# Optimization experiments

Measured on AMD Instinct MI355X. Metric: run time of the kernel, lower is better.

Reference implementation:

```python
import jax, jax.numpy as jnp
import numpy as np

NQ = 4          # QUANTUM_QUBITS
DIM = 2 ** NQ   # 16-dim statevector
N_LAYERS = 2
BATCH = 1 << 20


def _bit(idx, w):
    # PennyLane convention: wire 0 is the most-significant bit
    return (idx >> (NQ - 1 - w)) & 1

# Precompute CNOT permutations for the ring (w, (w+1)%NQ): flip target bit when control bit is 1.
_CNOT_PERMS = []
for w in range(NQ):
    c, t = w, (w + 1) % NQ
    perm = np.arange(DIM)
    for idx in range(DIM):
        if _bit(idx, c):
            perm[idx] = idx ^ (1 << (NQ - 1 - t))
    _CNOT_PERMS.append(jnp.asarray(perm))

# Z expectation sign vectors: sign = +1 if bit==0 else -1, per wire -> (NQ, DIM)
_Z_SIGNS = jnp.asarray(
    np.stack([[1.0 - 2.0 * _bit(idx, w) for idx in range(DIM)] for w in range(NQ)]),
    dtype=jnp.float32,
)


def _ry(t):
    c, s = jnp.cos(t / 2), jnp.sin(t / 2)
    return jnp.stack([jnp.stack([c, -s], -1), jnp.stack([s, c], -1)], -2).astype(jnp.complex64)


def _rx(t):
    c = jnp.cos(t / 2).astype(jnp.complex64)
    s = (-1j * jnp.sin(t / 2)).astype(jnp.complex64)
    return jnp.stack([jnp.stack([c, s], -1), jnp.stack([s, c], -1)], -2)


def _rz(t):
    em = jnp.exp(-0.5j * t.astype(jnp.complex64))
    ep = jnp.exp(0.5j * t.astype(jnp.complex64))
    zero = jnp.zeros_like(em)
    return jnp.stack([jnp.stack([em, zero], -1), jnp.stack([zero, ep], -1)], -2)


def _apply_batched(state, g, w):
    # state: (B, DIM); g: (B, 2, 2) per-sample gate on wire w
    s = state.reshape((-1,) + (2,) * NQ)
    s = jnp.moveaxis(s, 1 + w, 1)
    s = jnp.einsum('bij,bj...->bi...', g, s)
    s = jnp.moveaxis(s, 1, 1 + w)
    return s.reshape(-1, DIM)


def _apply_shared(state, g, w):
    # state: (B, DIM); g: (2, 2) shared gate on wire w
    s = state.reshape((-1,) + (2,) * NQ)
    s = jnp.moveaxis(s, 1 + w, 1)
    s = jnp.einsum('ij,bj...->bi...', g, s)
    s = jnp.moveaxis(s, 1, 1 + w)
    return s.reshape(-1, DIM)


def setup_inputs() -> dict:
    key = jax.random.key(0)
    kx, kw = jax.random.split(key)
    x = jax.random.normal(kx, (BATCH, NQ), dtype=jnp.float32)
    weights = jax.random.normal(kw, (N_LAYERS, NQ, 3), dtype=jnp.float32) * 0.1
    return {"x": x, "weights": weights}


def reference(x, weights):
    B = x.shape[0]
    state = jnp.zeros((B, DIM), dtype=jnp.complex64).at[:, 0].set(1.0)
    # Angle embedding: RY(x_w) on each wire (per-sample gates)
    for w in range(NQ):
        state = _apply_batched(state, _ry(x[:, w]), w)
    # Variational layers: RX, RY, RZ per wire, then CNOT ring
    for l in range(weights.shape[0]):
        for w in range(NQ):
            state = _apply_shared(state, _rx(weights[l, w, 0]), w)
            state = _apply_shared(state, _ry(weights[l, w, 1]), w)
            state = _apply_shared(state, _rz(weights[l, w, 2]), w)
        for w in range(NQ):
            state = state[:, _CNOT_PERMS[w]]
    probs = (state.real ** 2 + state.imag ** 2)  # (B, DIM)
    return probs @ _Z_SIGNS.T  # (B, NQ) <Z_w> expvals
```

## Files before the change

kernel.cpp:

```cpp
#include <hip/hip_runtime.h>

#define NQ 4
#define DIM 16
#define SPT 4

struct cplx { float r, i; };
__device__ inline cplx cmul(cplx a, cplx b) { return {a.r*b.r - a.i*b.i, a.r*b.i + a.i*b.r}; }
__device__ inline cplx cadd(cplx a, cplx b) { return {a.r + b.r, a.i + b.i}; }

__device__ inline void build9(float u, float v, float* t) {
    float su, cu, sv, cv;
    __sincosf(u, &su, &cu);
    __sincosf(v, &sv, &cv);
    t[0] = 1.f;      t[1] = cv;      t[2] = sv;
    t[3] = cu;       t[4] = cu * cv; t[5] = cu * sv;
    t[6] = su;       t[7] = su * cv; t[8] = su * sv;
}

__global__ __launch_bounds__(256) void qsim_kernel(const float4* __restrict__ x,
                                                   const float* __restrict__ wt,
                                                   float4* __restrict__ out, int quarter) {
    __shared__ float Ur[DIM][DIM];
    __shared__ float Ui[DIM][DIM];
    __shared__ float A[4][DIM][DIM];
    __shared__ float4 lk[81];

    int tid = blockIdx.x * blockDim.x + threadIdx.x;
    bool valid = tid < quarter;
    float4 xs[SPT];
#pragma unroll
    for (int s = 0; s < SPT; ++s)
        xs[s] = valid ? x[tid + s * quarter] : make_float4(0.f, 0.f, 0.f, 0.f);

    int col = threadIdx.x;
    if (col < DIM) {
        float ar[DIM], ai[DIM];
#pragma unroll
        for (int i = 0; i < DIM; ++i) { ar[i] = 0.f; ai[i] = 0.f; }
        ar[col] = 1.f;
        for (int l = 0; l < 2; ++l) {
            for (int q = 0; q < NQ; ++q) {
                float tx = wt[(l * 4 + q) * 3 + 0];
                float ty = wt[(l * 4 + q) * 3 + 1];
                float tz = wt[(l * 4 + q) * 3 + 2];
                float cx, sx, cy, sy, cz, sz;
                __sincosf(0.5f * tx, &sx, &cx);
                __sincosf(0.5f * ty, &sy, &cy);
                __sincosf(0.5f * tz, &sz, &cz);
                cplx Rx[2][2] = {{{cx, 0.f}, {0.f, -sx}}, {{0.f, -sx}, {cx, 0.f}}};
                cplx Ry[2][2] = {{{cy, 0.f}, {-sy, 0.f}}, {{sy, 0.f}, {cy, 0.f}}};
                cplx Rz[2][2] = {{{cz, -sz}, {0.f, 0.f}}, {{0.f, 0.f}, {cz, sz}}};
                cplx T[2][2], G[2][2];
#pragma unroll
                for (int r = 0; r < 2; ++r)
#pragma unroll
                    for (int c = 0; c < 2; ++c)
                        T[r][c] = cadd(cmul(Ry[r][0], Rx[0][c]), cmul(Ry[r][1], Rx[1][c]));
#pragma unroll
                for (int r = 0; r < 2; ++r)
#pragma unroll
                    for (int c = 0; c < 2; ++c)
                        G[r][c] = cadd(cmul(Rz[r][0], T[0][c]), cmul(Rz[r][1], T[1][c]));
                int pos = 3 - q, mask = 1 << pos;
#pragma unroll
                for (int idx = 0; idx < DIM; ++idx) {
                    if (idx & mask) continue;
                    int i1 = idx | mask;
                    cplx a0 = {ar[idx], ai[idx]}, a1 = {ar[i1], ai[i1]};
                    cplx n0 = cadd(cmul(G[0][0], a0), cmul(G[0][1], a1));
                    cplx n1 = cadd(cmul(G[1][0], a0), cmul(G[1][1], a1));
                    ar[idx] = n0.r; ai[idx] = n0.i;
                    ar[i1] = n1.r;  ai[i1] = n1.i;
                }
            }
            for (int q = 0; q < NQ; ++q) {
                int cpos = 3 - q, tpos = 3 - ((q + 1) & 3);
                int tmask = 1 << tpos;
#pragma unroll
                for (int idx = 0; idx < DIM; ++idx) {
                    if (((idx >> cpos) & 1) && !((idx >> tpos) & 1)) {
                        int i1 = idx | tmask;
                        float tr = ar[idx]; ar[idx] = ar[i1]; ar[i1] = tr;
                        float ti = ai[idx]; ai[idx] = ai[i1]; ai[i1] = ti;
                    }
                }
            }
        }
        for (int i = 0; i < DIM; ++i) { Ur[i][col] = ar[i]; Ui[i][col] = ai[i]; }
    }
    __syncthreads();

    {
        int j = threadIdx.x >> 4, k = threadIdx.x & 15;
        float a0 = 0.f, a1 = 0.f, a2 = 0.f, a3 = 0.f;
#pragma unroll
        for (int idx = 0; idx < DIM; ++idx) {
            float rr = Ur[idx][j] * Ur[idx][k] + Ui[idx][j] * Ui[idx][k];
            a0 += (idx & 8) ? -rr : rr;
            a1 += (idx & 4) ? -rr : rr;
            a2 += (idx & 2) ? -rr : rr;
            a3 += (idx & 1) ? -rr : rr;
        }
        A[0][j][k] = a0; A[1][j][k] = a1; A[2][j][k] = a2; A[3][j][k] = a3;
    }
    __syncthreads();

    for (int id = threadIdx.x; id < 4 * 81; id += blockDim.x) {
        int w = id & 3, u = id >> 2;
        int e0 = u / 27, e1 = (u / 9) % 3, e2 = (u / 3) % 3, e3 = u % 3;
        int m  = ((e0 == 2) ? 8 : 0) | ((e1 == 2) ? 4 : 0) | ((e2 == 2) ? 2 : 0) | ((e3 == 2) ? 1 : 0);
        int d1 = ((e0 == 1) ? 8 : 0) | ((e1 == 1) ? 4 : 0) | ((e2 == 1) ? 2 : 0) | ((e3 == 1) ? 1 : 0);
        float acc = 0.f;
#pragma unroll
        for (int b = 0; b < DIM; ++b) {
            float sgn = (__popc(b & d1) & 1) ? -1.f : 1.f;
            acc += sgn * A[w][b][b ^ m];
        }
        ((float*)lk)[u * 4 + w] = 0.0625f * acc;
    }
    __syncthreads();

    if (!valid) return;
    float t9[SPT][9], u9[SPT][9];
#pragma unroll
    for (int s = 0; s < SPT; ++s) {
        build9(xs[s].x, xs[s].y, t9[s]);
        build9(xs[s].z, xs[s].w, u9[s]);
    }

    float4 acc[SPT];
#pragma unroll
    for (int s = 0; s < SPT; ++s) acc[s] = make_float4(0.f, 0.f, 0.f, 0.f);

#pragma unroll
    for (int i = 0; i < 9; ++i) {
#pragma unroll
        for (int j = 0; j < 9; ++j) {
            float4 c = lk[i * 9 + j];
#pragma unroll
            for (int s = 0; s < SPT; ++s) {
                float p = t9[s][i] * u9[s][j];
                acc[s].x = fmaf(c.x, p, acc[s].x);
                acc[s].y = fmaf(c.y, p, acc[s].y);
                acc[s].z = fmaf(c.z, p, acc[s].z);
                acc[s].w = fmaf(c.w, p, acc[s].w);
            }
        }
    }
#pragma unroll
    for (int s = 0; s < SPT; ++s)
        out[tid + s * quarter] = acc[s];
}

extern "C" void kernel_launch(void* const* d_in, const int* in_sizes, int n_in,
                              void* d_out, int out_size, void* d_ws, size_t ws_size,
                              hipStream_t stream) {
    const float* x = (const float*)d_in[0];
    const float* wt = (const float*)d_in[1];
    float* out = (float*)d_out;
    (void)d_ws; (void)ws_size;

    int B = in_sizes[0] / NQ;
    int quarter = B / SPT;
    int blocks = (quarter + 255) / 256;
    qsim_kernel<<<blocks, 256, 0, stream>>>((const float4*)x, wt, (float4*)out, quarter);
}
```

Measured before the change: 81.58 us.

## Split coefficient setup into single-block kernel, contract kernel reads precomputed table

Before, every block re-simulated the 16x16 variational unitary and rebuilt the 81x4 coefficient table in shared memory. Now a one-block setup kernel writes the table to workspace once, and the batched contraction kernel just loads it into shared memory. This removes redundant per-block setup work and two barriers. In exchange it adds a second kernel launch and a global round trip for the table. The loops are also turned into compile-time unrolls via a template helper.

```diff
diff --git a/kernel.cpp b/kernel.cpp
--- a/kernel.cpp
+++ b/kernel.cpp
@@ -8,7 +8,12 @@
 __device__ inline cplx cmul(cplx a, cplx b) { return {a.r*b.r - a.i*b.i, a.r*b.i + a.i*b.r}; }
 __device__ inline cplx cadd(cplx a, cplx b) { return {a.r + b.r, a.i + b.i}; }
 
-__device__ inline void build9(float u, float v, float* t) {
+template<int I> struct ic { static constexpr int v = I; };
+template<int N, typename F> __device__ __forceinline__ void sfor(F f) {
+    if constexpr (N > 0) { sfor<N - 1>(f); f(ic<N - 1>{}); }
+}
+
+__device__ __forceinline__ void build9(float u, float v, float* t) {
     float su, cu, sv, cv;
     __sincosf(u, &su, &cu);
     __sincosf(v, &sv, &cv);
@@ -17,20 +22,11 @@
     t[6] = su;       t[7] = su * cv; t[8] = su * sv;
 }
 
-__global__ __launch_bounds__(256) void qsim_kernel(const float4* __restrict__ x,
-                                                   const float* __restrict__ wt,
-                                                   float4* __restrict__ out, int quarter) {
+__global__ __launch_bounds__(256) void setup_kernel(const float* __restrict__ wt,
+                                                    float* __restrict__ gk) {
     __shared__ float Ur[DIM][DIM];
     __shared__ float Ui[DIM][DIM];
     __shared__ float A[4][DIM][DIM];
-    __shared__ float4 lk[81];
-
-    int tid = blockIdx.x * blockDim.x + threadIdx.x;
-    bool valid = tid < quarter;
-    float4 xs[SPT];
-#pragma unroll
-    for (int s = 0; s < SPT; ++s)
-        xs[s] = valid ? x[tid + s * quarter] : make_float4(0.f, 0.f, 0.f, 0.f);
 
     int col = threadIdx.x;
     if (col < DIM) {
@@ -38,7 +34,9 @@
 #pragma unroll
         for (int i = 0; i < DIM; ++i) { ar[i] = 0.f; ai[i] = 0.f; }
         ar[col] = 1.f;
+#pragma unroll
         for (int l = 0; l < 2; ++l) {
+#pragma unroll
             for (int q = 0; q < NQ; ++q) {
                 float tx = wt[(l * 4 + q) * 3 + 0];
                 float ty = wt[(l * 4 + q) * 3 + 1];
@@ -73,6 +71,7 @@
                     ar[i1] = n1.r;  ai[i1] = n1.i;
                 }
             }
+#pragma unroll
             for (int q = 0; q < NQ; ++q) {
                 int cpos = 3 - q, tpos = 3 - ((q + 1) & 3);
                 int tmask = 1 << tpos;
@@ -86,6 +85,7 @@
                 }
             }
         }
+#pragma unroll
         for (int i = 0; i < DIM; ++i) { Ur[i][col] = ar[i]; Ui[i][col] = ai[i]; }
     }
     __syncthreads();
@@ -116,40 +116,50 @@
             float sgn = (__popc(b & d1) & 1) ? -1.f : 1.f;
             acc += sgn * A[w][b][b ^ m];
         }
-        ((float*)lk)[u * 4 + w] = 0.0625f * acc;
+        gk[u * 4 + w] = 0.0625f * acc;
     }
+}
+
+__global__ __launch_bounds__(256) void contract_kernel(const float4* __restrict__ x,
+                                                       const float4* __restrict__ gk,
+                                                       float4* __restrict__ out, int quarter) {
+    __shared__ float4 lk[81];
+
+    int tid = blockIdx.x * blockDim.x + threadIdx.x;
+    bool valid = tid < quarter;
+
+    float4 xs[SPT];
+    sfor<SPT>([&](auto S) {
+        xs[S.v] = valid ? x[tid + S.v * quarter] : make_float4(0.f, 0.f, 0.f, 0.f);
+    });
+
+    if (threadIdx.x < 81) lk[threadIdx.x] = gk[threadIdx.x];
     __syncthreads();
 
-    if (!valid) return;
     float t9[SPT][9], u9[SPT][9];
-#pragma unroll
-    for (int s = 0; s < SPT; ++s) {
-        build9(xs[s].x, xs[s].y, t9[s]);
-        build9(xs[s].z, xs[s].w, u9[s]);
-    }
+    sfor<SPT>([&](auto S) {
+        build9(xs[S.v].x, xs[S.v].y, t9[S.v]);
+        build9(xs[S.v].z, xs[S.v].w, u9[S.v]);
+    });
 
     float4 acc[SPT];
-#pragma unroll
-    for (int s = 0; s < SPT; ++s) acc[s] = make_float4(0.f, 0.f, 0.f, 0.f);
+    sfor<SPT>([&](auto S) { acc[S.v] = make_float4(0.f, 0.f, 0.f, 0.f); });
 
-#pragma unroll
-    for (int i = 0; i < 9; ++i) {
-#pragma unroll
-        for (int j = 0; j < 9; ++j) {
-            float4 c = lk[i * 9 + j];
-#pragma unroll
-            for (int s = 0; s < SPT; ++s) {
-                float p = t9[s][i] * u9[s][j];
-                acc[s].x = fmaf(c.x, p, acc[s].x);
-                acc[s].y = fmaf(c.y, p, acc[s].y);
-                acc[s].z = fmaf(c.z, p, acc[s].z);
-                acc[s].w = fmaf(c.w, p, acc[s].w);
-            }
-        }
-    }
-#pragma unroll
-    for (int s = 0; s < SPT; ++s)
-        out[tid + s * quarter] = acc[s];
+    sfor<9>([&](auto I) {
+        sfor<9>([&](auto J) {
+            float4 c = lk[I.v * 9 + J.v];
+            sfor<SPT>([&](auto S) {
+                float p = t9[S.v][I.v] * u9[S.v][J.v];
+                acc[S.v].x = fmaf(c.x, p, acc[S.v].x);
+                acc[S.v].y = fmaf(c.y, p, acc[S.v].y);
+                acc[S.v].z = fmaf(c.z, p, acc[S.v].z);
+                acc[S.v].w = fmaf(c.w, p, acc[S.v].w);
+            });
+        });
+    });
+
+    if (!valid) return;
+    sfor<SPT>([&](auto S) { out[tid + S.v * quarter] = acc[S.v]; });
 }
 
 extern "C" void kernel_launch(void* const* d_in, const int* in_sizes, int n_in,
@@ -158,10 +168,14 @@
     const float* x = (const float*)d_in[0];
     const float* wt = (const float*)d_in[1];
     float* out = (float*)d_out;
-    (void)d_ws; (void)ws_size;
+    float* gk = (float*)d_ws;
+    (void)ws_size; (void)n_in; (void)out_size;
 
     int B = in_sizes[0] / NQ;
     int quarter = B / SPT;
     int blocks = (quarter + 255) / 256;
-    qsim_kernel<<<blocks, 256, 0, stream>>>((const float4*)x, wt, (float4*)out, quarter);
+
+    setup_kernel<<<1, 256, 0, stream>>>(wt, gk);
+    contract_kernel<<<blocks, 256, 0, stream>>>((const float4*)x, (const float4*)gk,
+                                                (float4*)out, quarter);
 }
```

Result: slower. 85.24 us (+4.5%).
